# Kernel tuning notes

Measured on AMD Instinct MI355X. Metric: run time of the kernel, lower is better.

## Reference

```python
import jax, jax.numpy as jnp
import numpy as np

N_EMBD = 1024
HEAD_SIZE = 64

def setup_inputs() -> dict:
    key = jax.random.key(0)
    kx, kk, kq, kv = jax.random.split(key, 4)
    x = jax.random.normal(kx, (8, 2048, N_EMBD), dtype=jnp.float32)
    scale = 1.0 / np.sqrt(N_EMBD)
    # nn.Linear weights are [out, in]; kaiming-uniform-ish init
    Wk = jax.random.uniform(kk, (HEAD_SIZE, N_EMBD), dtype=jnp.float32, minval=-scale, maxval=scale)
    Wq = jax.random.uniform(kq, (HEAD_SIZE, N_EMBD), dtype=jnp.float32, minval=-scale, maxval=scale)
    Wv = jax.random.uniform(kv, (HEAD_SIZE, N_EMBD), dtype=jnp.float32, minval=-scale, maxval=scale)
    return {"x": x, "Wk": Wk, "Wq": Wq, "Wv": Wv}

def reference(x, Wk, Wq, Wv):
    # x: [B, T, E]; W*: [H, E] (torch Linear layout)
    k = jnp.einsum('bte,he->bth', x, Wk)
    q = jnp.einsum('bte,he->bth', x, Wq)
    v = jnp.einsum('bte,he->bth', x, Wv)
    inv_sqrt_h = 1.0 / np.sqrt(HEAD_SIZE)
    wei = jnp.einsum('bth,bsh->bts', q, k) * inv_sqrt_h  # [B, T, T]
    wei = jax.nn.softmax(wei, axis=-1)
    out = jnp.einsum('bts,bsh->bth', wei, v)  # [B, T, H]
    return out
```

## Files before the change

### kernel.cpp

```cpp
#include <hip/hip_runtime.h>
#include <cstdint>

#define NB 8
#define TS 2048
#define NE 1024
#define HD 64
#define MTOT (NB*TS)

typedef float     f4  __attribute__((ext_vector_type(4)));
typedef short     s8v __attribute__((ext_vector_type(8)));
typedef short     s4v __attribute__((ext_vector_type(4)));
typedef int       i4v __attribute__((ext_vector_type(4)));
typedef _Float16  h8  __attribute__((ext_vector_type(8)));

__device__ __forceinline__ short f2bf(float f) {
  union { float f; uint32_t u; } x; x.f = f;
  return (short)((x.u + 0x7FFFu + ((x.u >> 16) & 1u)) >> 16);
}

__device__ __forceinline__ int pack2(float lo, float hi) {
  union { float f; uint32_t u; } a, b; a.f = lo; b.f = hi;
  return (int)__builtin_amdgcn_perm(b.u + 0x8000u, a.u + 0x8000u, 0x07060302u);
}

__device__ __forceinline__ void gl2lds(const void* gptr, void* lptr) {
  auto g = (const __attribute__((address_space(1))) uint32_t*)gptr;
  auto l = (__attribute__((address_space(3))) uint32_t*)lptr;
  __builtin_amdgcn_global_load_lds(g, l, 16, 0, 0);
}

template <int N>
__device__ __forceinline__ void wait_barrier() {
  asm volatile("s_waitcnt vmcnt(%0) lgkmcnt(0)" :: "n"(N) : "memory");
  __builtin_amdgcn_s_barrier();
}

__global__ __launch_bounds__(256) void wconv_kernel(
    const float* __restrict__ Wk, const float* __restrict__ Wq, const float* __restrict__ Wv,
    short* __restrict__ wb)
{
  const int idx = (blockIdx.x * 256 + threadIdx.x) * 4;
  const int p = idx >> 16;
  const int off = idx & 65535;
  const float* W = (p == 0) ? Wq : (p == 1) ? Wk : Wv;
  const float s = (p == 0) ? 0.18033688011112042f : 1.0f;
  const float4 v = *(const float4*)&W[off];
  s4v h; h[0] = f2bf(v.x*s); h[1] = f2bf(v.y*s); h[2] = f2bf(v.z*s); h[3] = f2bf(v.w*s);
  *(s4v*)&wb[idx] = h;
}

__global__ __launch_bounds__(256) void proj_kernel(
    const float* __restrict__ x, const short* __restrict__ wb,
    short* __restrict__ qo, short* __restrict__ ko, _Float16* __restrict__ vo)
{
  __shared__ float Xs[4][32][64];
  __shared__ short Ws[2][192][64];
  const int tid = threadIdx.x;
  const int wv = tid >> 6, lane = tid & 63, n = lane & 15, quad = lane >> 4;
  const int mg = wv & 1, cg = wv >> 1;
  const int r0 = blockIdx.x * 32;
  const int xrow = lane >> 4, xslot = lane & 15;
  const int wrow = lane >> 3, wslot = lane & 7;

  auto dmaX = [&](int c, int buf) {
#pragma unroll
    for (int u = 0; u < 2; ++u) {
      const int R0 = (wv * 2 + u) * 4;
      const int row = R0 + xrow;
      const int gs = (xslot + row) & 15;
      gl2lds(&x[(size_t)(r0 + row) * NE + c * 64 + gs * 4], &Xs[buf][R0][0]);
    }
  };
  auto dmaW = [&](int c, int buf) {
#pragma unroll
    for (int u = 0; u < 6; ++u) {
      const int C0 = (wv * 6 + u) * 8;
      const int col = C0 + wrow;
      const int gs = (wslot + col) & 7;
      gl2lds(&wb[(size_t)col * NE + c * 64 + gs * 8], &Ws[buf][C0][0]);
    }
  };

  const f4 fz = {0.f, 0.f, 0.f, 0.f};
  f4 acc[6] = {fz, fz, fz, fz, fz, fz};

  auto compute = [&](int bw, int bx) {
    s8v a[2];
    const int row = mg * 16 + n;
#pragma unroll
    for (int kc = 0; kc < 2; ++kc) {
      const int u0 = kc * 8 + quad * 2;
      const float* pr = &Xs[bx][row][0];
      const f4 f0 = *(const f4*)(pr + (((u0    ) - row) & 15) * 4);
      const f4 f1 = *(const f4*)(pr + (((u0 + 1) - row) & 15) * 4);
      i4v ai;
      ai[0] = pack2(f0[0], f0[1]); ai[1] = pack2(f0[2], f0[3]);
      ai[2] = pack2(f1[0], f1[1]); ai[3] = pack2(f1[2], f1[3]);
      a[kc] = __builtin_bit_cast(s8v, ai);
    }
#pragma unroll
    for (int nf = 0; nf < 6; ++nf) {
      const int col = cg * 96 + nf * 16 + n;
      const s8v b0 = *(const s8v*)&Ws[bw][col][(((0 + quad) - col) & 7) * 8];
      const s8v b1 = *(const s8v*)&Ws[bw][col][(((4 + quad) - col) & 7) * 8];
      acc[nf] = __builtin_amdgcn_mfma_f32_16x16x32_bf16(a[0], b0, acc[nf], 0, 0, 0);
      acc[nf] = __builtin_amdgcn_mfma_f32_16x16x32_bf16(a[1], b1, acc[nf], 0, 0, 0);
    }
  };

  dmaW(0, 0); dmaX(0, 0); dmaX(1, 1); dmaX(2, 2);
  wait_barrier<4>();

  for (int t = 0; t < 16; ++t) {
    if (t <= 14) dmaW(t + 1, (t + 1) & 1);
    if (t <= 12) dmaX(t + 3, (t + 3) & 3);
    compute(t & 1, t & 3);
    if (t <= 12)      wait_barrier<2>();
    else if (t <= 14) wait_barrier<0>();
  }

#pragma unroll
  for (int nf = 0; nf < 6; ++nf) {
    const int gc = cg * 96 + nf * 16;
    const int p = gc >> 6;
    const int rcol = (gc & 63) + n;
#pragma unroll
    for (int i = 0; i < 4; ++i) {
      const int R = r0 + mg * 16 + quad * 4 + i;
      const float av = acc[nf][i];
      if (p == 0)      qo[(size_t)R * HD + rcol] = f2bf(av);
      else if (p == 1) ko[(size_t)R * HD + rcol] = f2bf(av);
      else {
        const int t2 = R & (TS - 1), b = t2 & 31;
        const int pos = (t2 & ~31) | (((b >> 2) & 3) << 3) | (((b >> 4) & 1) << 2) | (b & 3);
        vo[(size_t)(R >> 11) * HD * TS + (size_t)rcol * TS + pos] = (_Float16)av;
      }
    }
  }
}

__global__ __launch_bounds__(512) void attn_kernel(
    const short* __restrict__ q, const short* __restrict__ k,
    const _Float16* __restrict__ vT, float* __restrict__ out)
{
  __shared__ __align__(16) char smem[98304];
  const int tid = threadIdx.x;
  const int wv = tid >> 6, lane = tid & 63, n = lane & 15, quad = lane >> 4;
  const int half = wv >> 2, qw = wv & 3;
  const int batch = blockIdx.x & 7;
  const int qg = blockIdx.x >> 3;
  const int m0 = batch * TS + qg * 64;
  const short*    kb = k  + (size_t)batch * TS * HD;
  const _Float16* vb = vT + (size_t)batch * HD * TS;
  const int drow = lane >> 3, dslot = lane & 7;
  const f4 fz = {0.f, 0.f, 0.f, 0.f};

  auto kbuf = [&](int buf) { return (short*)   (smem +         (half * 3 + buf) * 8192); };
  auto vbuf = [&](int buf) { return (_Float16*)(smem + 49152 + (half * 3 + buf) * 8192); };

  auto dmaKV = [&](int tt, int buf) {
    const int c = half * 16 + tt;
#pragma unroll
    for (int u = 0; u < 2; ++u) {
      const int K0 = (qw * 2 + u) * 8;
      const int key = K0 + drow;
      const int gs = (dslot + key) & 7;
      gl2lds(&kb[(size_t)(c * 64 + key) * HD + gs * 8], kbuf(buf) + K0 * 64);
    }
#pragma unroll
    for (int u = 0; u < 2; ++u) {
      const int D0 = (qw * 2 + u) * 8;
      const int d = D0 + drow;
      const int gs = (dslot + d) & 7;
      gl2lds(&vb[(size_t)d * TS + c * 64 + gs * 8], vbuf(buf) + D0 * 64);
    }
  };

  s8v qf[2];
#pragma unroll
  for (int kc = 0; kc < 2; ++kc)
    qf[kc] = *(const s8v*)&q[(size_t)(m0 + qw * 16 + n) * HD + kc * 32 + quad * 8];

  f4 o[4] = {fz, fz, fz, fz};
  f4 lD = fz;
  h8 ones;
#pragma unroll
  for (int j = 0; j < 8; ++j) ones[j] = (_Float16)1.0f;

  dmaKV(0, 0); dmaKV(1, 1);
  wait_barrier<4>();

  for (int t = 0; t < 16; ++t) {
    const int buf = t % 3;
    if (t <= 13) dmaKV(t + 2, (t + 2) % 3);

    const short*    ks = kbuf(buf);
    const _Float16* vs = vbuf(buf);

    s8v kf[4][2];
#pragma unroll
    for (int f = 0; f < 4; ++f)
#pragma unroll
      for (int kc = 0; kc < 2; ++kc) {
        const int key = f * 16 + n;
        kf[f][kc] = *(const s8v*)&ks[key * 64 + (((kc * 4 + quad) - key) & 7) * 8];
      }

    f4 st[4];
#pragma unroll
    for (int f = 0; f < 4; ++f) {
      st[f] = __builtin_amdgcn_mfma_f32_16x16x32_bf16(kf[f][0], qf[0], fz, 0, 0, 0);
      st[f] = __builtin_amdgcn_mfma_f32_16x16x32_bf16(kf[f][1], qf[1], st[f], 0, 0, 0);
    }

    h8 pa[2];
#pragma unroll
    for (int pr = 0; pr < 2; ++pr)
#pragma unroll
      for (int hf = 0; hf < 2; ++hf)
#pragma unroll
        for (int i = 0; i < 4; ++i)
          pa[pr][hf * 4 + i] = (_Float16)__builtin_amdgcn_exp2f(st[pr * 2 + hf][i]);

#pragma unroll
    for (int pr = 0; pr < 2; ++pr) {
      lD = __builtin_amdgcn_mfma_f32_16x16x32_f16(pa[pr], ones, lD, 0, 0, 0);
#pragma unroll
      for (int g = 0; g < 4; ++g) {
        const int d = g * 16 + n;
        const h8 vf = *(const h8*)&vs[d * 64 + (((pr * 4 + quad) - d) & 7) * 8];
        o[g] = __builtin_amdgcn_mfma_f32_16x16x32_f16(pa[pr], vf, o[g], 0, 0, 0);
      }
    }

    if (t <= 13)      wait_barrier<4>();
    else if (t == 14) wait_barrier<0>();
  }

  __syncthreads();

  float* o_c = (float*)smem;
  float* l_c = (float*)(smem + 36864);
  if (n == 0)
#pragma unroll
    for (int i = 0; i < 4; ++i) l_c[wv * 16 + quad * 4 + i] = lD[i];
#pragma unroll
  for (int g = 0; g < 4; ++g)
#pragma unroll
    for (int i = 0; i < 4; ++i)
      o_c[(wv * 16 + quad * 4 + i) * 68 + g * 16 + n] = o[g][i];
  __syncthreads();

#pragma unroll
  for (int rep = 0; rep < 2; ++rep) {
    const int idx = tid + rep * 512;
    const int qr = idx >> 4, d4 = (idx & 15) * 4;
    const int qw2 = qr >> 4, wr = qr & 15;
    const float L = l_c[qw2 * 16 + wr] + l_c[(qw2 + 4) * 16 + wr];
    const f4 s0 = *(const f4*)&o_c[(qw2 * 16 + wr) * 68 + d4];
    const f4 s1 = *(const f4*)&o_c[((qw2 + 4) * 16 + wr) * 68 + d4];
    f4 r = (s0 + s1);
    const float inv = 1.0f / L;
    r[0] *= inv; r[1] *= inv; r[2] *= inv; r[3] *= inv;
    *(f4*)&out[(size_t)(m0 + qr) * HD + d4] = r;
  }
}

extern "C" void kernel_launch(void* const* d_in, const int* in_sizes, int n_in,
                              void* d_out, int out_size, void* d_ws, size_t ws_size,
                              hipStream_t stream) {
  const float* x  = (const float*)d_in[0];
  const float* Wk = (const float*)d_in[1];
  const float* Wq = (const float*)d_in[2];
  const float* Wv = (const float*)d_in[3];
  float* out = (float*)d_out;

  short* qb = (short*)d_ws;
  short* kb = qb + (size_t)MTOT * HD;
  _Float16* vb = (_Float16*)(kb + (size_t)MTOT * HD);
  short* wb = (short*)(vb + (size_t)NB * HD * TS);

  wconv_kernel<<<192, 256, 0, stream>>>(Wk, Wq, Wv, wb);
  proj_kernel<<<MTOT / 32, 256, 0, stream>>>(x, wb, qb, kb, vb);
  attn_kernel<<<MTOT / 64, 512, 0, stream>>>(qb, kb, vb, out);
}
```

Baseline: 129.4 us.

## Split attention keys four ways per block and load V fragments directly from global

Each block's eight waves are reorganised from two key-halves by four query strips into four key-quarters by two query strips of 32 rows. Each wave now processes 32 queries, so every K and V fragment is reused across two query sub-tiles. V is no longer staged through LDS and is read straight from global memory into registers. Only K is double-buffered in LDS, and the final reduction sums four partial outputs. This raises MFMA reuse per load and halves LDS traffic, at the cost of more registers and uncoalesced global V reads that may stall.

```diff
diff --git a/kernel.cpp b/kernel.cpp
--- a/kernel.cpp
+++ b/kernel.cpp
@@ -146,57 +146,58 @@
   __shared__ __align__(16) char smem[98304];
   const int tid = threadIdx.x;
   const int wv = tid >> 6, lane = tid & 63, n = lane & 15, quad = lane >> 4;
-  const int half = wv >> 2, qw = wv & 3;
+  const int kq = wv & 3, qg = wv >> 2;
   const int batch = blockIdx.x & 7;
-  const int qg = blockIdx.x >> 3;
-  const int m0 = batch * TS + qg * 64;
+  const int qgb = blockIdx.x >> 3;
+  const int m0 = batch * TS + qgb * 64;
   const short*    kb = k  + (size_t)batch * TS * HD;
   const _Float16* vb = vT + (size_t)batch * HD * TS;
   const int drow = lane >> 3, dslot = lane & 7;
   const f4 fz = {0.f, 0.f, 0.f, 0.f};
 
-  auto kbuf = [&](int buf) { return (short*)   (smem +         (half * 3 + buf) * 8192); };
-  auto vbuf = [&](int buf) { return (_Float16*)(smem + 49152 + (half * 3 + buf) * 8192); };
-
-  auto dmaKV = [&](int tt, int buf) {
-    const int c = half * 16 + tt;
-#pragma unroll
-    for (int u = 0; u < 2; ++u) {
-      const int K0 = (qw * 2 + u) * 8;
+  auto kbuf = [&](int buf) { return (short*)(smem + (kq * 3 + buf) * 8192); };
+
+  auto dmaK = [&](int tt, int buf) {
+    const int c = kq * 8 + tt;
+#pragma unroll
+    for (int u = 0; u < 4; ++u) {
+      const int K0 = (qg * 4 + u) * 8;
       const int key = K0 + drow;
       const int gs = (dslot + key) & 7;
       gl2lds(&kb[(size_t)(c * 64 + key) * HD + gs * 8], kbuf(buf) + K0 * 64);
     }
-#pragma unroll
-    for (int u = 0; u < 2; ++u) {
-      const int D0 = (qw * 2 + u) * 8;
-      const int d = D0 + drow;
-      const int gs = (dslot + d) & 7;
-      gl2lds(&vb[(size_t)d * TS + c * 64 + gs * 8], vbuf(buf) + D0 * 64);
-    }
-  };
-
-  s8v qf[2];
-#pragma unroll
-  for (int kc = 0; kc < 2; ++kc)
-    qf[kc] = *(const s8v*)&q[(size_t)(m0 + qw * 16 + n) * HD + kc * 32 + quad * 8];
-
-  f4 o[4] = {fz, fz, fz, fz};
-  f4 lD = fz;
+  };
+
+  s8v qf[2][2];
+#pragma unroll
+  for (int qh = 0; qh < 2; ++qh)
+#pragma unroll
+    for (int kc = 0; kc < 2; ++kc)
+      qf[qh][kc] = *(const s8v*)&q[(size_t)(m0 + qg * 32 + qh * 16 + n) * HD + kc * 32 + quad * 8];
+
+  f4 o[2][4] = {{fz, fz, fz, fz}, {fz, fz, fz, fz}};
+  f4 lD[2] = {fz, fz};
   h8 ones;
 #pragma unroll
   for (int j = 0; j < 8; ++j) ones[j] = (_Float16)1.0f;
 
-  dmaKV(0, 0); dmaKV(1, 1);
+  dmaK(0, 0); dmaK(1, 1);
   wait_barrier<4>();
 
-  for (int t = 0; t < 16; ++t) {
+  for (int t = 0; t < 8; ++t) {
     const int buf = t % 3;
-    if (t <= 13) dmaKV(t + 2, (t + 2) % 3);
-
-    const short*    ks = kbuf(buf);
-    const _Float16* vs = vbuf(buf);
-
+    const int c = kq * 8 + t;
+
+    h8 vfr[2][4];
+#pragma unroll
+    for (int pr = 0; pr < 2; ++pr)
+#pragma unroll
+      for (int g = 0; g < 4; ++g)
+        vfr[pr][g] = *(const h8*)&vb[(size_t)(g * 16 + n) * TS + c * 64 + (pr * 4 + quad) * 8];
+
+    if (t <= 5) dmaK(t + 2, (t + 2) % 3);
+
+    const short* ks = kbuf(buf);
     s8v kf[4][2];
 #pragma unroll
     for (int f = 0; f < 4; ++f)
@@ -206,60 +207,72 @@
         kf[f][kc] = *(const s8v*)&ks[key * 64 + (((kc * 4 + quad) - key) & 7) * 8];
       }
 
-    f4 st[4];
-#pragma unroll
-    for (int f = 0; f < 4; ++f) {
-      st[f] = __builtin_amdgcn_mfma_f32_16x16x32_bf16(kf[f][0], qf[0], fz, 0, 0, 0);
-      st[f] = __builtin_amdgcn_mfma_f32_16x16x32_bf16(kf[f][1], qf[1], st[f], 0, 0, 0);
-    }
-
-    h8 pa[2];
-#pragma unroll
-    for (int pr = 0; pr < 2; ++pr)
-#pragma unroll
-      for (int hf = 0; hf < 2; ++hf)
-#pragma unroll
-        for (int i = 0; i < 4; ++i)
-          pa[pr][hf * 4 + i] = (_Float16)__builtin_amdgcn_exp2f(st[pr * 2 + hf][i]);
+    f4 st[2][4];
+#pragma unroll
+    for (int qh = 0; qh < 2; ++qh)
+#pragma unroll
+      for (int f = 0; f < 4; ++f) {
+        st[qh][f] = __builtin_amdgcn_mfma_f32_16x16x32_bf16(kf[f][0], qf[qh][0], fz, 0, 0, 0);
+        st[qh][f] = __builtin_amdgcn_mfma_f32_16x16x32_bf16(kf[f][1], qf[qh][1], st[qh][f], 0, 0, 0);
+      }
+
+    h8 pa[2][2];
+#pragma unroll
+    for (int qh = 0; qh < 2; ++qh)
+#pragma unroll
+      for (int pr = 0; pr < 2; ++pr)
+#pragma unroll
+        for (int hf = 0; hf < 2; ++hf)
+#pragma unroll
+          for (int i = 0; i < 4; ++i)
+            pa[qh][pr][hf * 4 + i] = (_Float16)__builtin_amdgcn_exp2f(st[qh][pr * 2 + hf][i]);
 
 #pragma unroll
     for (int pr = 0; pr < 2; ++pr) {
-      lD = __builtin_amdgcn_mfma_f32_16x16x32_f16(pa[pr], ones, lD, 0, 0, 0);
-#pragma unroll
-      for (int g = 0; g < 4; ++g) {
-        const int d = g * 16 + n;
-        const h8 vf = *(const h8*)&vs[d * 64 + (((pr * 4 + quad) - d) & 7) * 8];
-        o[g] = __builtin_amdgcn_mfma_f32_16x16x32_f16(pa[pr], vf, o[g], 0, 0, 0);
-      }
-    }
-
-    if (t <= 13)      wait_barrier<4>();
-    else if (t == 14) wait_barrier<0>();
+#pragma unroll
+      for (int qh = 0; qh < 2; ++qh)
+        lD[qh] = __builtin_amdgcn_mfma_f32_16x16x32_f16(pa[qh][pr], ones, lD[qh], 0, 0, 0);
+#pragma unroll
+      for (int g = 0; g < 4; ++g)
+#pragma unroll
+        for (int qh = 0; qh < 2; ++qh)
+          o[qh][g] = __builtin_amdgcn_mfma_f32_16x16x32_f16(pa[qh][pr], vfr[pr][g], o[qh][g], 0, 0, 0);
+    }
+
+    if (t <= 5)      wait_barrier<4>();
+    else if (t == 6) wait_barrier<0>();
   }
 
   __syncthreads();
 
   float* o_c = (float*)smem;
-  float* l_c = (float*)(smem + 36864);
+  float* l_c = (float*)(smem + 69632);
   if (n == 0)
 #pragma unroll
-    for (int i = 0; i < 4; ++i) l_c[wv * 16 + quad * 4 + i] = lD[i];
-#pragma unroll
-  for (int g = 0; g < 4; ++g)
-#pragma unroll
-    for (int i = 0; i < 4; ++i)
-      o_c[(wv * 16 + quad * 4 + i) * 68 + g * 16 + n] = o[g][i];
+    for (int qh = 0; qh < 2; ++qh)
+#pragma unroll
+      for (int i = 0; i < 4; ++i)
+        l_c[kq * 64 + qg * 32 + qh * 16 + quad * 4 + i] = lD[qh][i];
+#pragma unroll
+  for (int qh = 0; qh < 2; ++qh)
+#pragma unroll
+    for (int g = 0; g < 4; ++g)
+#pragma unroll
+      for (int i = 0; i < 4; ++i)
+        o_c[kq * 4352 + (qg * 32 + qh * 16 + quad * 4 + i) * 68 + g * 16 + n] = o[qh][g][i];
   __syncthreads();
 
 #pragma unroll
   for (int rep = 0; rep < 2; ++rep) {
     const int idx = tid + rep * 512;
     const int qr = idx >> 4, d4 = (idx & 15) * 4;
-    const int qw2 = qr >> 4, wr = qr & 15;
-    const float L = l_c[qw2 * 16 + wr] + l_c[(qw2 + 4) * 16 + wr];
-    const f4 s0 = *(const f4*)&o_c[(qw2 * 16 + wr) * 68 + d4];
-    const f4 s1 = *(const f4*)&o_c[((qw2 + 4) * 16 + wr) * 68 + d4];
-    f4 r = (s0 + s1);
+    float L = 0.f;
+    f4 r = fz;
+#pragma unroll
+    for (int c2 = 0; c2 < 4; ++c2) {
+      L += l_c[c2 * 64 + qr];
+      r += *(const f4*)&o_c[c2 * 4352 + qr * 68 + d4];
+    }
     const float inv = 1.0f / L;
     r[0] *= inv; r[1] *= inv; r[2] *= inv; r[3] *= inv;
     *(f4*)&out[(size_t)(m0 + qr) * HD + d4] = r;
```

Measured after the change: 139.7 us. 1.08x slower.
